# Kernel optimization log

Hardware: AMD Instinct MI355X
Metric: run time of the kernel (lower is better)

Reference implementation:

```python
import jax, jax.numpy as jnp
import numpy as np

GN_GROUPS = 32
GN_EPS = 1e-5
K = 3  # deform kernel size, padding=1, dilation=1


def conv1x1(x, w):  # x [B,C,H,W], w [O,C]
    return jnp.einsum('bchw,oc->bohw', x, w)


def conv3x3(x, w):  # w [O,I,3,3], stride 1, pad 1
    return jax.lax.conv_general_dilated(
        x, w, window_strides=(1, 1), padding=((1, 1), (1, 1)),
        dimension_numbers=('NCHW', 'OIHW', 'NCHW'))


def group_norm(x, gamma, beta):
    B, C, H, W = x.shape
    xg = x.reshape(B, GN_GROUPS, C // GN_GROUPS, H, W)
    mu = xg.mean(axis=(2, 3, 4), keepdims=True)
    var = xg.var(axis=(2, 3, 4), keepdims=True)
    xn = ((xg - mu) * jax.lax.rsqrt(var + GN_EPS)).reshape(B, C, H, W)
    return xn * gamma[None, :, None, None] + beta[None, :, None, None]


def deform_conv(x, offset, w):
    """DeformConv v1, kernel 3, pad 1, deformable_groups=1.
    x [B,C,H,W]; offset [B,18,H,W] as (dy,dx) per kernel tap; w [O,C,3,3]."""
    B, C, H, W = x.shape
    off = offset.reshape(B, K * K, 2, H, W)
    dy, dx = off[:, :, 0], off[:, :, 1]                      # [B,9,H,W]
    ky, kx = jnp.meshgrid(jnp.arange(K) - 1, jnp.arange(K) - 1, indexing='ij')
    ky = ky.reshape(1, K * K, 1, 1).astype(x.dtype)
    kx = kx.reshape(1, K * K, 1, 1).astype(x.dtype)
    gy = jnp.arange(H, dtype=x.dtype).reshape(1, 1, H, 1)
    gx = jnp.arange(W, dtype=x.dtype).reshape(1, 1, 1, W)
    py = gy + ky + dy                                        # [B,9,H,W] sample y
    px = gx + kx + dx                                        # [B,9,H,W] sample x

    y0 = jnp.floor(py); x0 = jnp.floor(px)
    wy1 = py - y0; wy0 = 1.0 - wy1
    wx1 = px - x0; wx0 = 1.0 - wx1
    xf = x.reshape(B, C, H * W)

    def corner(yc, xc, wgt):
        valid = (yc >= 0) & (yc < H) & (xc >= 0) & (xc < W)  # zero padding outside
        yi = jnp.clip(yc, 0, H - 1).astype(jnp.int32)
        xi = jnp.clip(xc, 0, W - 1).astype(jnp.int32)
        idx = (yi * W + xi).reshape(B, -1)                   # [B, 9*H*W]
        v = jax.vmap(lambda f, i: f[:, i])(xf, idx)          # [B, C, 9*H*W]
        v = v.reshape(B, C, K * K, H, W)
        return v * (wgt * valid.astype(x.dtype))[:, None]

    sampled = (corner(y0, x0, wy0 * wx0) + corner(y0, x0 + 1, wy0 * wx1)
               + corner(y0 + 1, x0, wy1 * wx0) + corner(y0 + 1, x0 + 1, wy1 * wx1))
    # contract sampled [B,C,9,H,W] with weights [O,C,9]
    return jnp.einsum('bckhw,ock->bohw', sampled, w.reshape(w.shape[0], C, K * K))


def setup_inputs() -> dict:
    key = jax.random.key(0)
    ks = jax.random.split(key, 8)
    B, Cc, H, W = 4, 256, 128, 128
    ci = Cc // 4  # 64
    x = jax.random.normal(ks[0], (B, Cc, H, W), dtype=jnp.float32)
    w1 = jax.random.normal(ks[1], (ci, Cc), dtype=jnp.float32) * 0.05
    g1 = jnp.ones((ci,), jnp.float32); b1 = jnp.zeros((ci,), jnp.float32)
    w_off = jax.random.normal(ks[2], (18, ci, 3, 3), dtype=jnp.float32) * 0.01
    w_def = jax.random.normal(ks[3], (ci, ci, 3, 3), dtype=jnp.float32) * 0.05
    w3 = jax.random.normal(ks[4], (Cc, ci), dtype=jnp.float32) * 0.05
    g3 = jnp.ones((Cc,), jnp.float32); b3 = jnp.zeros((Cc,), jnp.float32)
    return {'x': x, 'w1': w1, 'g1': g1, 'b1': b1, 'w_off': w_off,
            'w_def': w_def, 'w3': w3, 'g3': g3, 'b3': b3}


def reference(x, w1, g1, b1, w_off, w_def, w3, g3, b3):
    xd = jax.nn.relu(group_norm(conv1x1(x, w1), g1, b1))     # scale1
    offset1 = conv3x3(xd, w_off)                              # off_conva
    out1 = deform_conv(xd, offset1, w_def)                    # kernel_conva
    out = out1 + xd
    out = jax.nn.relu(group_norm(conv1x1(out, w3), g3, b3)) + x  # scale3 + residual
    return out
```

## Files before the change

### kernel.cpp

```cpp
#include <hip/hip_runtime.h>


#define HW 16384
#define WIDTH 128

typedef __attribute__((ext_vector_type(8))) short bf16x8;
typedef __attribute__((ext_vector_type(4))) float f32x4;

__device__ __forceinline__ unsigned short f2bf(float f) {
  unsigned int u = __float_as_uint(f);
  u = (u + 0x7fffu + ((u >> 16) & 1u)) >> 16;
  return (unsigned short)u;
}
__device__ __forceinline__ float bflo(unsigned int u) { return __uint_as_float(u << 16); }
__device__ __forceinline__ float bfhi(unsigned int u) { return __uint_as_float(u & 0xffff0000u); }

__global__ __launch_bounds__(256) void k_prep(const float* __restrict__ w1, const float* __restrict__ w3,
                                              const float* __restrict__ wdef, const float* __restrict__ woff,
                                              unsigned short* __restrict__ wA1f,
                                              unsigned short* __restrict__ wBf,
                                              unsigned short* __restrict__ wofBf,
                                              unsigned short* __restrict__ w3Bf) {
  int i = blockIdx.x * 256 + threadIdx.x;
  if (i < 16384) {
    int j = i & 7;
    int lane = (i >> 3) & 63;
    int m = (i >> 9) & 3;
    int kt = i >> 11;
    int o = (m << 4) + (lane & 15);
    int c = kt * 32 + ((lane >> 4) << 3) + j;
    wA1f[i] = f2bf(w1[(size_t)o * 256 + c]);
  }
  if (i < 36864) {
    int j = i & 7;
    int lane = (i >> 3) & 63;
    int n = (i >> 9) & 3;
    int kt = i >> 11;
    int kk = kt * 32 + ((lane >> 4) << 3) + j;
    int tap = kk >> 6, c = kk & 63;
    int o = (n << 4) + (lane & 15);
    wBf[i] = f2bf(wdef[(size_t)o * 576 + c * 9 + tap]);
  }
  if (i < 18432) {
    int j = i & 7;
    int lane = (i >> 3) & 63;
    int n = (i >> 9) & 1;
    int kt = i >> 10;
    int kk = kt * 32 + ((lane >> 4) << 3) + j;
    int tap = kk >> 6, c = kk & 63;
    int o = (n << 4) + (lane & 15);
    wofBf[i] = (o < 18) ? f2bf(woff[((size_t)(o * 64 + c)) * 9 + tap]) : (unsigned short)0;
  }
  if (i < 32768) {
    int j = i & 7;
    int lane = (i >> 3) & 63;
    int n = (i >> 9) & 15;
    int kt = i >> 13;
    int c = kt * 32 + ((lane >> 4) << 3) + j;
    int o = (n << 4) + (lane & 15);
    w3Bf[i] = f2bf(w3[(size_t)o * 64 + c]);
  }
}

__global__ __launch_bounds__(256) void k_conv1m(const float* __restrict__ x,
                                                const unsigned short* __restrict__ wA1f,
                                                unsigned short* __restrict__ xdT, float* __restrict__ ps) {
  __shared__ unsigned short xs[64][72];
  __shared__ float lds_s[4][32], lds_ss[4][32];
  int tid = threadIdx.x;
  int wave = tid >> 6, lane = tid & 63;
  int b = blockIdx.x >> 8;
  int chunk = blockIdx.x & 255;
  int px0 = chunk << 6;
  int pxl = lane & 15, q = lane >> 4;
  const float* xb = x + (size_t)b * 256 * HW + px0;
  const bf16x8* wAp = (const bf16x8*)wA1f;
  f32x4 acc[4];
#pragma unroll
  for (int m = 0; m < 4; m++) acc[m] = (f32x4){0.f, 0.f, 0.f, 0.f};

  for (int cb = 0; cb < 4; cb++) {
    __syncthreads();
#pragma unroll
    for (int r = 0; r < 4; r++) {
      int idx = r * 256 + tid;
      int c = idx >> 4;
      int qd = idx & 15;
      float4 v = *(const float4*)(xb + (size_t)(cb * 64 + c) * HW + qd * 4);
      xs[qd * 4 + 0][c] = f2bf(v.x);
      xs[qd * 4 + 1][c] = f2bf(v.y);
      xs[qd * 4 + 2][c] = f2bf(v.z);
      xs[qd * 4 + 3][c] = f2bf(v.w);
    }
    __syncthreads();
#pragma unroll
    for (int kt = 0; kt < 2; kt++) {
      bf16x8 bfrag = *(const bf16x8*)&xs[wave * 16 + pxl][kt * 32 + q * 8];
      int ktG = cb * 2 + kt;
#pragma unroll
      for (int m = 0; m < 4; m++) {
        bf16x8 af = wAp[(ktG * 4 + m) * 64 + lane];
        acc[m] = __builtin_amdgcn_mfma_f32_16x16x32_bf16(af, bfrag, acc[m], 0, 0, 0);
      }
    }
  }
  unsigned short* xo = xdT + ((size_t)b * HW + px0 + wave * 16 + pxl) * 64 + (q << 2);
#pragma unroll
  for (int m = 0; m < 4; m++) {
    unsigned int u0, u1;
    asm("v_cvt_pk_bf16_f32 %0, %1, %2" : "=v"(u0) : "v"(acc[m][0]), "v"(acc[m][1]));
    asm("v_cvt_pk_bf16_f32 %0, %1, %2" : "=v"(u1) : "v"(acc[m][2]), "v"(acc[m][3]));
    *(uint2*)(xo + m * 16) = make_uint2(u0, u1);
  }
  float s[8], sq[8];
#pragma unroll
  for (int m = 0; m < 4; m++)
#pragma unroll
    for (int h = 0; h < 2; h++) {
      float a = acc[m][2 * h] + acc[m][2 * h + 1];
      float qq = acc[m][2 * h] * acc[m][2 * h] + acc[m][2 * h + 1] * acc[m][2 * h + 1];
      s[m * 2 + h] = a; sq[m * 2 + h] = qq;
    }
#pragma unroll
  for (int i = 0; i < 8; i++) {
#pragma unroll
    for (int off = 8; off; off >>= 1) {
      s[i] += __shfl_down(s[i], off, 16);
      sq[i] += __shfl_down(sq[i], off, 16);
    }
  }
  if (pxl == 0) {
#pragma unroll
    for (int i = 0; i < 8; i++) {
      int m = i >> 1, h = i & 1;
      int g = m * 8 + q * 2 + h;
      lds_s[wave][g] = s[i];
      lds_ss[wave][g] = sq[i];
    }
  }
  __syncthreads();
  if (tid < 32) {
    float S = lds_s[0][tid] + lds_s[1][tid] + lds_s[2][tid] + lds_s[3][tid];
    float SS = lds_ss[0][tid] + lds_ss[1][tid] + lds_ss[2][tid] + lds_ss[3][tid];
    int bg = b * 32 + tid;
    ps[(bg * 256 + chunk) * 2] = S;
    ps[(bg * 256 + chunk) * 2 + 1] = SS;
  }
}

__global__ __launch_bounds__(256) void k_gnfin_p(const float* __restrict__ ps, float* __restrict__ mrs,
                                                 int S, float n) {
  int bg = blockIdx.x;
  float s = 0.f, ss = 0.f;
  for (int i = threadIdx.x; i < S; i += 256) { s += ps[(bg * S + i) * 2]; ss += ps[(bg * S + i) * 2 + 1]; }
#pragma unroll
  for (int off = 32; off; off >>= 1) { s += __shfl_down(s, off); ss += __shfl_down(ss, off); }
  __shared__ float ls[4], lss[4];
  int wv = threadIdx.x >> 6;
  if ((threadIdx.x & 63) == 0) { ls[wv] = s; lss[wv] = ss; }
  __syncthreads();
  if (threadIdx.x == 0) {
    float Sa = ls[0] + ls[1] + ls[2] + ls[3];
    float SSa = lss[0] + lss[1] + lss[2] + lss[3];
    float mu = Sa / n;
    float var = SSa / n - mu * mu;
    mrs[bg] = mu;
    mrs[128 + bg] = rsqrtf(var + 1e-5f);
  }
}

__global__ __launch_bounds__(256) void k_gnapply_bf(unsigned short* __restrict__ xdT,
                                                    const float* __restrict__ mrs,
                                                    const float* __restrict__ g1, const float* __restrict__ b1) {
  int i = blockIdx.x * 256 + threadIdx.x;
  int b = i >> 17;
  int ck = i & 7;
  int c0 = ck << 3;
  uint4 v = ((const uint4*)xdT)[i];
  float ga[8], be[8];
#pragma unroll
  for (int j = 0; j < 8; j += 2) {
    int g = (c0 + j) >> 1;
    float mu = mrs[b * 32 + g], rs = mrs[128 + b * 32 + g];
    ga[j] = g1[c0 + j] * rs;     be[j] = b1[c0 + j] - mu * ga[j];
    ga[j + 1] = g1[c0 + j + 1] * rs; be[j + 1] = b1[c0 + j + 1] - mu * ga[j + 1];
  }
  float r[8];
  r[0] = fmaxf(bflo(v.x) * ga[0] + be[0], 0.f);
  r[1] = fmaxf(bfhi(v.x) * ga[1] + be[1], 0.f);
  r[2] = fmaxf(bflo(v.y) * ga[2] + be[2], 0.f);
  r[3] = fmaxf(bfhi(v.y) * ga[3] + be[3], 0.f);
  r[4] = fmaxf(bflo(v.z) * ga[4] + be[4], 0.f);
  r[5] = fmaxf(bfhi(v.z) * ga[5] + be[5], 0.f);
  r[6] = fmaxf(bflo(v.w) * ga[6] + be[6], 0.f);
  r[7] = fmaxf(bfhi(v.w) * ga[7] + be[7], 0.f);
  uint4 o;
  asm("v_cvt_pk_bf16_f32 %0, %1, %2" : "=v"(o.x) : "v"(r[0]), "v"(r[1]));
  asm("v_cvt_pk_bf16_f32 %0, %1, %2" : "=v"(o.y) : "v"(r[2]), "v"(r[3]));
  asm("v_cvt_pk_bf16_f32 %0, %1, %2" : "=v"(o.z) : "v"(r[4]), "v"(r[5]));
  asm("v_cvt_pk_bf16_f32 %0, %1, %2" : "=v"(o.w) : "v"(r[6]), "v"(r[7]));
  ((uint4*)xdT)[i] = o;
}

__global__ __launch_bounds__(576, 7) void k_mega(const unsigned short* __restrict__ xdT,
                                                 const unsigned short* __restrict__ wofBf,
                                                 const unsigned short* __restrict__ wBf,
                                                 const unsigned short* __restrict__ w3Bf,
                                                 unsigned short* __restrict__ t3,
                                                 float* __restrict__ ps2) {
  __shared__ unsigned short A[36 * 65 * 8];
  __shared__ float offsL[64 * 18];
  int tid = threadIdx.x;
  int bb = blockIdx.x >> 8;
  int tileid = blockIdx.x & 255;
  int px0 = tileid << 6;
  const unsigned short* xtf = xdT + (size_t)bb * 64 * HW;
  const char* xbt = (const char*)xtf;
  int wave = tid >> 6;
  int lane = tid & 63;
  int q16 = lane >> 2;
  int ch4 = lane & 3;
  int kcbyte = (wave * 4 + ch4) * 1040;
  int kq = lane >> 4;

  f32x4 aoff = {0.f, 0.f, 0.f, 0.f};
  {
    int ky = wave / 3 - 1, kx = wave % 3 - 1;
    int n2 = wave & 1;
    int mh1 = wave >> 1;
    int r1 = mh1 * 16 + (lane & 15);
    for (int h = 0; h < 2; ++h) {
      int co = (h << 6) + (ch4 << 4);
#pragma unroll
      for (int g = 0; g < 4; ++g) {
        int src = (g << 4) + q16;
        int px = px0 + src;
        int sy = (px >> 7) + ky;
        int sx = (px & 127) + kx;
        bool valid = ((unsigned)sy < 128u) && ((unsigned)sx < 128u);
        uint4 v = make_uint4(0u, 0u, 0u, 0u);
        if (valid) v = *(const uint4*)(xbt + (((sy << 7) + sx) << 7) + co);
        *(uint4*)((char*)A + kcbyte + src * 16) = v;
      }
      __syncthreads();
      if (wave < 8) {
        const bf16x8* wp = (const bf16x8*)wofBf;
        __builtin_amdgcn_s_setprio(1);
#pragma unroll
        for (int tap = 0; tap < 9; ++tap) {
          bf16x8 bk = wp[((2 * tap + h) * 2 + n2) * 64 + lane];
          bf16x8 a0 = *(const bf16x8*)((const char*)A + ((tap * 4 + kq) * 65 + r1) * 16);
          aoff = __builtin_amdgcn_mfma_f32_16x16x32_bf16(a0, bk, aoff, 0, 0, 0);
        }
        __builtin_amdgcn_s_setprio(0);
      }
      __syncthreads();
    }
    if (wave < 8) {
      int o = n2 * 16 + (lane & 15);
      if (o < 18) {
        int prow = mh1 * 16 + ((lane >> 4) << 2);
#pragma unroll
        for (int r = 0; r < 4; r++) offsL[(prow + r) * 18 + o] = aoff[r];
      }
    }
  }
  __syncthreads();

  float w00, w01, w10, w11;
  int a00, a01, a10, a11;
  {
    int px = px0 + lane;
    int y = px >> 7, xc = px & 127;
    float dy = offsL[lane * 18 + 2 * wave];
    float dx = offsL[lane * 18 + 2 * wave + 1];
    float py = (float)(y + wave / 3 - 1) + dy;
    float pxx = (float)(xc + wave % 3 - 1) + dx;
    float y0f = floorf(py), x0f = floorf(pxx);
    float ay = py - y0f, ax = pxx - x0f;
    int y0 = (int)y0f, x0 = (int)x0f;
    int y1i = y0 + 1, x1i = x0 + 1;
    float by0 = 1.f - ay, bx0 = 1.f - ax;
    bool vy0 = (unsigned)y0 < 128u, vy1 = (unsigned)y1i < 128u;
    bool vx0 = (unsigned)x0 < 128u, vx1 = (unsigned)x1i < 128u;
    w00 = (vy0 && vx0) ? by0 * bx0 : 0.f;
    w01 = (vy0 && vx1) ? by0 * ax : 0.f;
    w10 = (vy1 && vx0) ? ay * bx0 : 0.f;
    w11 = (vy1 && vx1) ? ay * ax : 0.f;
    int iy0 = min(max(y0, 0), 127), iy1 = min(max(y1i, 0), 127);
    int ix0 = min(max(x0, 0), 127), ix1 = min(max(x1i, 0), 127);
    a00 = (iy0 * WIDTH + ix0) << 7;
    a01 = (iy0 * WIDTH + ix1) << 7;
    a10 = (iy1 * WIDTH + ix0) << 7;
    a11 = (iy1 * WIDTH + ix1) << 7;
  }

  int n1 = wave & 3;
  int mh = wave >> 2;
  f32x4 acc0 = {0.f, 0.f, 0.f, 0.f};
  f32x4 acc1 = {0.f, 0.f, 0.f, 0.f};
  for (int h = 0; h < 2; ++h) {
    int co = (h << 6) + (ch4 << 4);
#pragma unroll
    for (int g = 0; g < 4; ++g) {
      int src = (g << 4) + q16;
      float j0 = __shfl(w00, src), j1 = __shfl(w01, src);
      float j2 = __shfl(w10, src), j3 = __shfl(w11, src);
      int b0 = __shfl(a00, src), b1 = __shfl(a01, src);
      int b2 = __shfl(a10, src), b3 = __shfl(a11, src);
      uint4 v0 = *(const uint4*)(xbt + b0 + co);
      uint4 v1 = *(const uint4*)(xbt + b1 + co);
      uint4 v2 = *(const uint4*)(xbt + b2 + co);
      uint4 v3 = *(const uint4*)(xbt + b3 + co);
      float r[8];
      r[0] = j0 * bflo(v0.x) + j1 * bflo(v1.x) + j2 * bflo(v2.x) + j3 * bflo(v3.x);
      r[1] = j0 * bfhi(v0.x) + j1 * bfhi(v1.x) + j2 * bfhi(v2.x) + j3 * bfhi(v3.x);
      r[2] = j0 * bflo(v0.y) + j1 * bflo(v1.y) + j2 * bflo(v2.y) + j3 * bflo(v3.y);
      r[3] = j0 * bfhi(v0.y) + j1 * bfhi(v1.y) + j2 * bfhi(v2.y) + j3 * bfhi(v3.y);
      r[4] = j0 * bflo(v0.z) + j1 * bflo(v1.z) + j2 * bflo(v2.z) + j3 * bflo(v3.z);
      r[5] = j0 * bfhi(v0.z) + j1 * bfhi(v1.z) + j2 * bfhi(v2.z) + j3 * bfhi(v3.z);
      r[6] = j0 * bflo(v0.w) + j1 * bflo(v1.w) + j2 * bflo(v2.w) + j3 * bflo(v3.w);
      r[7] = j0 * bfhi(v0.w) + j1 * bfhi(v1.w) + j2 * bfhi(v2.w) + j3 * bfhi(v3.w);
      uint4 ov;
      asm("v_cvt_pk_bf16_f32 %0, %1, %2" : "=v"(ov.x) : "v"(r[0]), "v"(r[1]));
      asm("v_cvt_pk_bf16_f32 %0, %1, %2" : "=v"(ov.y) : "v"(r[2]), "v"(r[3]));
      asm("v_cvt_pk_bf16_f32 %0, %1, %2" : "=v"(ov.z) : "v"(r[4]), "v"(r[5]));
      asm("v_cvt_pk_bf16_f32 %0, %1, %2" : "=v"(ov.w) : "v"(r[6]), "v"(r[7]));
      *(uint4*)((char*)A + kcbyte + src * 16) = ov;
    }
    __syncthreads();
    if (wave < 8) {
      int r0r = mh * 32 + (lane & 15);
      const bf16x8* wp = (const bf16x8*)wBf;
      __builtin_amdgcn_s_setprio(1);
#pragma unroll
      for (int tap = 0; tap < 9; ++tap) {
        bf16x8 bk = wp[((2 * tap + h) * 4 + n1) * 64 + lane];
        int kc = tap * 4 + kq;
        bf16x8 a0 = *(const bf16x8*)((const char*)A + (kc * 65 + r0r) * 16);
        bf16x8 a1 = *(const bf16x8*)((const char*)A + (kc * 65 + r0r + 16) * 16);
        acc0 = __builtin_amdgcn_mfma_f32_16x16x32_bf16(a0, bk, acc0, 0, 0, 0);
        acc1 = __builtin_amdgcn_mfma_f32_16x16x32_bf16(a1, bk, acc1, 0, 0, 0);
      }
      __builtin_amdgcn_s_setprio(0);
    }
    __syncthreads();
  }
  if (wave < 8) {
    int c = n1 * 16 + (lane & 15);
    int pb = px0 + mh * 32 + ((lane >> 4) << 2);
#pragma unroll
    for (int r = 0; r < 4; r++) {
      acc0[r] += __uint_as_float((unsigned int)xtf[(size_t)(pb + r) * 64 + c] << 16);
      acc1[r] += __uint_as_float((unsigned int)xtf[(size_t)(pb + 16 + r) * 64 + c] << 16);
    }
    char* base = (char*)A + (c >> 3) * 1040 + (c & 7) * 2;
    int pxr = mh * 32 + ((lane >> 4) << 2);
#pragma unroll
    for (int r = 0; r < 4; r++) {
      *(unsigned short*)(base + (size_t)(pxr + r) * 16) = f2bf(acc0[r]);
      *(unsigned short*)(base + (size_t)(pxr + 16 + r) * 16) = f2bf(acc1[r]);
    }
  }
  __syncthreads();
  if (wave >= 8) return;

  f32x4 cA[4], cB[4];
#pragma unroll
  for (int ni = 0; ni < 4; ni++) {
    cA[ni] = (f32x4){0.f, 0.f, 0.f, 0.f};
    cB[ni] = (f32x4){0.f, 0.f, 0.f, 0.f};
  }
  {
    int mt0 = (wave >> 2) * 2;
    const bf16x8* wp2 = (const bf16x8*)w3Bf;
    __builtin_amdgcn_s_setprio(1);
#pragma unroll
    for (int kt = 0; kt < 2; kt++) {
      int kc = kt * 4 + kq;
      bf16x8 aA = *(const bf16x8*)((const char*)A + (size_t)(kc * 65 + mt0 * 16 + (lane & 15)) * 16);
      bf16x8 aB = *(const bf16x8*)((const char*)A + (size_t)(kc * 65 + (mt0 + 1) * 16 + (lane & 15)) * 16);
#pragma unroll
      for (int ni = 0; ni < 4; ni++) {
        int ng = n1 * 4 + ni;
        bf16x8 bk = wp2[(kt * 16 + ng) * 64 + lane];
        cA[ni] = __builtin_amdgcn_mfma_f32_16x16x32_bf16(aA, bk, cA[ni], 0, 0, 0);
        cB[ni] = __builtin_amdgcn_mfma_f32_16x16x32_bf16(aB, bk, cB[ni], 0, 0, 0);
      }
    }
    __builtin_amdgcn_s_setprio(0);
  }
#pragma unroll
  for (int ni = 0; ni < 4; ni++) {
    float s = 0.f, qq = 0.f;
#pragma unroll
    for (int r = 0; r < 4; r++) {
      float v0 = cA[ni][r], v1 = cB[ni][r];
      s += v0 + v1; qq += v0 * v0 + v1 * v1;
    }
    s += __shfl_down(s, 32); qq += __shfl_down(qq, 32);
    s += __shfl_down(s, 16); qq += __shfl_down(qq, 16);
    s += __shfl_down(s, 4);  qq += __shfl_down(qq, 4);
    s += __shfl_down(s, 2);  qq += __shfl_down(qq, 2);
    s += __shfl_down(s, 1);  qq += __shfl_down(qq, 1);
    if (lane == 0 || lane == 8) {
      int g = (n1 * 4 + ni) * 2 + (lane >> 3);
      int slot = ((bb * 32 + g) * 256 + tileid) * 2 + (wave >> 2);
      ps2[slot * 2] = s;
      ps2[slot * 2 + 1] = qq;
    }
  }
  unsigned short* tb = t3 + (size_t)bb * 256 * HW + px0;
  int mtq = (wave >> 2) * 32 + ((lane >> 4) << 2);
#pragma unroll
  for (int ni = 0; ni < 4; ni++) {
    int o = (n1 * 4 + ni) * 16 + (lane & 15);
    unsigned short* p0 = tb + (size_t)o * HW + mtq;
    unsigned int u0, u1, u2, u3;
    asm("v_cvt_pk_bf16_f32 %0, %1, %2" : "=v"(u0) : "v"(cA[ni][0]), "v"(cA[ni][1]));
    asm("v_cvt_pk_bf16_f32 %0, %1, %2" : "=v"(u1) : "v"(cA[ni][2]), "v"(cA[ni][3]));
    asm("v_cvt_pk_bf16_f32 %0, %1, %2" : "=v"(u2) : "v"(cB[ni][0]), "v"(cB[ni][1]));
    asm("v_cvt_pk_bf16_f32 %0, %1, %2" : "=v"(u3) : "v"(cB[ni][2]), "v"(cB[ni][3]));
    *(uint2*)p0 = make_uint2(u0, u1);
    *(uint2*)(p0 + 16) = make_uint2(u2, u3);
  }
}

__global__ __launch_bounds__(256) void k_final(const unsigned short* __restrict__ t3, const float* __restrict__ x,
                                               const float* __restrict__ mrs, const float* __restrict__ g3,
                                               const float* __restrict__ b3, float* __restrict__ out) {
  int i4 = blockIdx.x * 256 + threadIdx.x;
  int b = i4 >> 20;
  int c = (i4 >> 12) & 255;
  int g = c >> 3;
  float mu = mrs[b * 32 + g], rs = mrs[128 + b * 32 + g];
  float ga = g3[c] * rs, be = b3[c] - mu * ga;
  uint2 tv = ((const uint2*)t3)[i4];
  float t0 = bflo(tv.x);
  float t1 = bfhi(tv.x);
  float t2 = bflo(tv.y);
  float t3v = bfhi(tv.y);
  float4 xv = ((const float4*)x)[i4];
  float4 r;
  r.x = fmaxf(t0 * ga + be, 0.f) + xv.x;
  r.y = fmaxf(t1 * ga + be, 0.f) + xv.y;
  r.z = fmaxf(t2 * ga + be, 0.f) + xv.z;
  r.w = fmaxf(t3v * ga + be, 0.f) + xv.w;
  ((float4*)out)[i4] = r;
}

extern "C" void kernel_launch(void* const* d_in, const int* in_sizes, int n_in,
                              void* d_out, int out_size, void* d_ws, size_t ws_size,
                              hipStream_t stream) {
  const float* x    = (const float*)d_in[0];
  const float* w1   = (const float*)d_in[1];
  const float* g1   = (const float*)d_in[2];
  const float* b1   = (const float*)d_in[3];
  const float* woff = (const float*)d_in[4];
  const float* wdef = (const float*)d_in[5];
  const float* w3   = (const float*)d_in[6];
  const float* g3   = (const float*)d_in[7];
  const float* b3   = (const float*)d_in[8];
  float* ws = (float*)d_ws;

  unsigned short* xdT = (unsigned short*)ws;
  unsigned short* t3  = (unsigned short*)(ws + 2097152);
  float* base = ws + 2097152 + 8388608;
  float* mrs1 = base;
  float* mrs2 = mrs1 + 256;
  unsigned short* wA1f  = (unsigned short*)(mrs2 + 256);
  unsigned short* wBf   = (unsigned short*)(mrs2 + 256 + 8192);
  unsigned short* wofBf = (unsigned short*)(mrs2 + 256 + 8192 + 18432);
  unsigned short* w3Bf  = (unsigned short*)(mrs2 + 256 + 8192 + 18432 + 9216);
  float* ps   = mrs2 + 256 + 8192 + 18432 + 9216 + 16384;
  float* ps2  = ps + 65536;
  float* out  = (float*)d_out;

  hipLaunchKernelGGL(k_prep, dim3(144), dim3(256), 0, stream, w1, w3, wdef, woff, wA1f, wBf, wofBf, w3Bf);
  hipLaunchKernelGGL(k_conv1m, dim3(1024), dim3(256), 0, stream, x, wA1f, xdT, ps);
  hipLaunchKernelGGL(k_gnfin_p, dim3(128), dim3(256), 0, stream, ps, mrs1, 256, (float)(2 * HW));
  hipLaunchKernelGGL(k_gnapply_bf, dim3(2048), dim3(256), 0, stream, xdT, mrs1, g1, b1);
  hipLaunchKernelGGL(k_mega, dim3(1024), dim3(576), 0, stream, xdT, wofBf, wBf, w3Bf, t3, ps2);
  hipLaunchKernelGGL(k_gnfin_p, dim3(128), dim3(256), 0, stream, ps2, mrs2, 512, 131072.f);
  hipLaunchKernelGGL(k_final, dim3(16384), dim3(256), 0, stream, t3, x, mrs2, g3, b3, out);
}
```

Baseline: 110.9 us.

## Fuse GroupNorm1 apply into mega kernel and double-buffer conv1 input staging

Removes the separate GroupNorm-apply pass over xdT and instead applies per-channel scale, shift and ReLU on the fly wherever the mega kernel reads xdT: the 3x3 offset-conv staging, the bilinear corner samples and the residual add. This drops one full read and write of the 4x16384x64 bf16 intermediate plus a kernel launch, at the cost of extra ALU work per gathered corner. Separately, k_conv1m now double-buffers its LDS tile and prefetches the next channel block into registers while MFMAs run, which removes one barrier per iteration but raises register and LDS usage.

New measurement: 127.2 us. 1.15x slower.

```diff
diff --git a/kernel.cpp b/kernel.cpp
--- a/kernel.cpp
+++ b/kernel.cpp
@@ -65,7 +65,7 @@
 __global__ __launch_bounds__(256) void k_conv1m(const float* __restrict__ x,
                                                 const unsigned short* __restrict__ wA1f,
                                                 unsigned short* __restrict__ xdT, float* __restrict__ ps) {
-  __shared__ unsigned short xs[64][72];
+  __shared__ unsigned short xs[2][64][72];
   __shared__ float lds_s[4][32], lds_ss[4][32];
   int tid = threadIdx.x;
   int wave = tid >> 6, lane = tid & 63;
@@ -75,27 +75,36 @@
   int pxl = lane & 15, q = lane >> 4;
   const float* xb = x + (size_t)b * 256 * HW + px0;
   const bf16x8* wAp = (const bf16x8*)wA1f;
+  int sc = tid >> 4;
+  int sq = tid & 15;
   f32x4 acc[4];
 #pragma unroll
   for (int m = 0; m < 4; m++) acc[m] = (f32x4){0.f, 0.f, 0.f, 0.f};
 
+  float4 vr[4];
+#pragma unroll
+  for (int r = 0; r < 4; r++)
+    vr[r] = *(const float4*)(xb + (size_t)(r * 16 + sc) * HW + sq * 4);
+#pragma unroll
+  for (int r = 0; r < 4; r++) {
+    int c = r * 16 + sc;
+    xs[0][sq * 4 + 0][c] = f2bf(vr[r].x);
+    xs[0][sq * 4 + 1][c] = f2bf(vr[r].y);
+    xs[0][sq * 4 + 2][c] = f2bf(vr[r].z);
+    xs[0][sq * 4 + 3][c] = f2bf(vr[r].w);
+  }
+  __syncthreads();
+
   for (int cb = 0; cb < 4; cb++) {
-    __syncthreads();
-#pragma unroll
-    for (int r = 0; r < 4; r++) {
-      int idx = r * 256 + tid;
-      int c = idx >> 4;
-      int qd = idx & 15;
-      float4 v = *(const float4*)(xb + (size_t)(cb * 64 + c) * HW + qd * 4);
-      xs[qd * 4 + 0][c] = f2bf(v.x);
-      xs[qd * 4 + 1][c] = f2bf(v.y);
-      xs[qd * 4 + 2][c] = f2bf(v.z);
-      xs[qd * 4 + 3][c] = f2bf(v.w);
-    }
-    __syncthreads();
+    int cur = cb & 1;
+    if (cb < 3) {
+#pragma unroll
+      for (int r = 0; r < 4; r++)
+        vr[r] = *(const float4*)(xb + (size_t)((cb + 1) * 64 + r * 16 + sc) * HW + sq * 4);
+    }
 #pragma unroll
     for (int kt = 0; kt < 2; kt++) {
-      bf16x8 bfrag = *(const bf16x8*)&xs[wave * 16 + pxl][kt * 32 + q * 8];
+      bf16x8 bfrag = *(const bf16x8*)&xs[cur][wave * 16 + pxl][kt * 32 + q * 8];
       int ktG = cb * 2 + kt;
 #pragma unroll
       for (int m = 0; m < 4; m++) {
@@ -103,6 +112,17 @@
         acc[m] = __builtin_amdgcn_mfma_f32_16x16x32_bf16(af, bfrag, acc[m], 0, 0, 0);
       }
     }
+    if (cb < 3) {
+#pragma unroll
+      for (int r = 0; r < 4; r++) {
+        int c = r * 16 + sc;
+        xs[cur ^ 1][sq * 4 + 0][c] = f2bf(vr[r].x);
+        xs[cur ^ 1][sq * 4 + 1][c] = f2bf(vr[r].y);
+        xs[cur ^ 1][sq * 4 + 2][c] = f2bf(vr[r].z);
+        xs[cur ^ 1][sq * 4 + 3][c] = f2bf(vr[r].w);
+      }
+    }
+    __syncthreads();
   }
   unsigned short* xo = xdT + ((size_t)b * HW + px0 + wave * 16 + pxl) * 64 + (q << 2);
 #pragma unroll
@@ -112,21 +132,21 @@
     asm("v_cvt_pk_bf16_f32 %0, %1, %2" : "=v"(u1) : "v"(acc[m][2]), "v"(acc[m][3]));
     *(uint2*)(xo + m * 16) = make_uint2(u0, u1);
   }
-  float s[8], sq[8];
+  float s[8], sq2[8];
 #pragma unroll
   for (int m = 0; m < 4; m++)
 #pragma unroll
     for (int h = 0; h < 2; h++) {
       float a = acc[m][2 * h] + acc[m][2 * h + 1];
       float qq = acc[m][2 * h] * acc[m][2 * h] + acc[m][2 * h + 1] * acc[m][2 * h + 1];
-      s[m * 2 + h] = a; sq[m * 2 + h] = qq;
+      s[m * 2 + h] = a; sq2[m * 2 + h] = qq;
     }
 #pragma unroll
   for (int i = 0; i < 8; i++) {
 #pragma unroll
     for (int off = 8; off; off >>= 1) {
       s[i] += __shfl_down(s[i], off, 16);
-      sq[i] += __shfl_down(sq[i], off, 16);
+      sq2[i] += __shfl_down(sq2[i], off, 16);
     }
   }
   if (pxl == 0) {
@@ -135,7 +155,7 @@
       int m = i >> 1, h = i & 1;
       int g = m * 8 + q * 2 + h;
       lds_s[wave][g] = s[i];
-      lds_ss[wave][g] = sq[i];
+      lds_ss[wave][g] = sq2[i];
     }
   }
   __syncthreads();
@@ -169,47 +189,18 @@
   }
 }
 
-__global__ __launch_bounds__(256) void k_gnapply_bf(unsigned short* __restrict__ xdT,
-                                                    const float* __restrict__ mrs,
-                                                    const float* __restrict__ g1, const float* __restrict__ b1) {
-  int i = blockIdx.x * 256 + threadIdx.x;
-  int b = i >> 17;
-  int ck = i & 7;
-  int c0 = ck << 3;
-  uint4 v = ((const uint4*)xdT)[i];
-  float ga[8], be[8];
-#pragma unroll
-  for (int j = 0; j < 8; j += 2) {
-    int g = (c0 + j) >> 1;
-    float mu = mrs[b * 32 + g], rs = mrs[128 + b * 32 + g];
-    ga[j] = g1[c0 + j] * rs;     be[j] = b1[c0 + j] - mu * ga[j];
-    ga[j + 1] = g1[c0 + j + 1] * rs; be[j + 1] = b1[c0 + j + 1] - mu * ga[j + 1];
-  }
-  float r[8];
-  r[0] = fmaxf(bflo(v.x) * ga[0] + be[0], 0.f);
-  r[1] = fmaxf(bfhi(v.x) * ga[1] + be[1], 0.f);
-  r[2] = fmaxf(bflo(v.y) * ga[2] + be[2], 0.f);
-  r[3] = fmaxf(bfhi(v.y) * ga[3] + be[3], 0.f);
-  r[4] = fmaxf(bflo(v.z) * ga[4] + be[4], 0.f);
-  r[5] = fmaxf(bfhi(v.z) * ga[5] + be[5], 0.f);
-  r[6] = fmaxf(bflo(v.w) * ga[6] + be[6], 0.f);
-  r[7] = fmaxf(bfhi(v.w) * ga[7] + be[7], 0.f);
-  uint4 o;
-  asm("v_cvt_pk_bf16_f32 %0, %1, %2" : "=v"(o.x) : "v"(r[0]), "v"(r[1]));
-  asm("v_cvt_pk_bf16_f32 %0, %1, %2" : "=v"(o.y) : "v"(r[2]), "v"(r[3]));
-  asm("v_cvt_pk_bf16_f32 %0, %1, %2" : "=v"(o.z) : "v"(r[4]), "v"(r[5]));
-  asm("v_cvt_pk_bf16_f32 %0, %1, %2" : "=v"(o.w) : "v"(r[6]), "v"(r[7]));
-  ((uint4*)xdT)[i] = o;
-}
-
 __global__ __launch_bounds__(576, 7) void k_mega(const unsigned short* __restrict__ xdT,
                                                  const unsigned short* __restrict__ wofBf,
                                                  const unsigned short* __restrict__ wBf,
                                                  const unsigned short* __restrict__ w3Bf,
+                                                 const float* __restrict__ mrs,
+                                                 const float* __restrict__ g1,
+                                                 const float* __restrict__ b1,
                                                  unsigned short* __restrict__ t3,
                                                  float* __restrict__ ps2) {
   __shared__ unsigned short A[36 * 65 * 8];
   __shared__ float offsL[64 * 18];
+  __shared__ float gnc[128];
   int tid = threadIdx.x;
   int bb = blockIdx.x >> 8;
   int tileid = blockIdx.x & 255;
@@ -223,6 +214,15 @@
   int kcbyte = (wave * 4 + ch4) * 1040;
   int kq = lane >> 4;
 
+  if (tid < 64) {
+    int c = tid, g = c >> 1;
+    float mu = mrs[bb * 32 + g], rs = mrs[128 + bb * 32 + g];
+    float ga = g1[c] * rs;
+    gnc[c] = ga;
+    gnc[64 + c] = b1[c] - mu * ga;
+  }
+  __syncthreads();
+
   f32x4 aoff = {0.f, 0.f, 0.f, 0.f};
   {
     int ky = wave / 3 - 1, kx = wave % 3 - 1;
@@ -230,6 +230,11 @@
     int mh1 = wave >> 1;
     int r1 = mh1 * 16 + (lane & 15);
     for (int h = 0; h < 2; ++h) {
+      int c0 = (h << 5) + (ch4 << 3);
+      float4 gA = *(const float4*)&gnc[c0];
+      float4 gB = *(const float4*)&gnc[c0 + 4];
+      float4 bA = *(const float4*)&gnc[64 + c0];
+      float4 bB = *(const float4*)&gnc[64 + c0 + 4];
       int co = (h << 6) + (ch4 << 4);
 #pragma unroll
       for (int g = 0; g < 4; ++g) {
@@ -240,7 +245,21 @@
         bool valid = ((unsigned)sy < 128u) && ((unsigned)sx < 128u);
         uint4 v = make_uint4(0u, 0u, 0u, 0u);
         if (valid) v = *(const uint4*)(xbt + (((sy << 7) + sx) << 7) + co);
-        *(uint4*)((char*)A + kcbyte + src * 16) = v;
+        float r[8];
+        r[0] = valid ? fmaxf(bflo(v.x) * gA.x + bA.x, 0.f) : 0.f;
+        r[1] = valid ? fmaxf(bfhi(v.x) * gA.y + bA.y, 0.f) : 0.f;
+        r[2] = valid ? fmaxf(bflo(v.y) * gA.z + bA.z, 0.f) : 0.f;
+        r[3] = valid ? fmaxf(bfhi(v.y) * gA.w + bA.w, 0.f) : 0.f;
+        r[4] = valid ? fmaxf(bflo(v.z) * gB.x + bB.x, 0.f) : 0.f;
+        r[5] = valid ? fmaxf(bfhi(v.z) * gB.y + bB.y, 0.f) : 0.f;
+        r[6] = valid ? fmaxf(bflo(v.w) * gB.z + bB.z, 0.f) : 0.f;
+        r[7] = valid ? fmaxf(bfhi(v.w) * gB.w + bB.w, 0.f) : 0.f;
+        uint4 ov;
+        asm("v_cvt_pk_bf16_f32 %0, %1, %2" : "=v"(ov.x) : "v"(r[0]), "v"(r[1]));
+        asm("v_cvt_pk_bf16_f32 %0, %1, %2" : "=v"(ov.y) : "v"(r[2]), "v"(r[3]));
+        asm("v_cvt_pk_bf16_f32 %0, %1, %2" : "=v"(ov.z) : "v"(r[4]), "v"(r[5]));
+        asm("v_cvt_pk_bf16_f32 %0, %1, %2" : "=v"(ov.w) : "v"(r[6]), "v"(r[7]));
+        *(uint4*)((char*)A + kcbyte + src * 16) = ov;
       }
       __syncthreads();
       if (wave < 8) {
@@ -300,27 +319,42 @@
   f32x4 acc0 = {0.f, 0.f, 0.f, 0.f};
   f32x4 acc1 = {0.f, 0.f, 0.f, 0.f};
   for (int h = 0; h < 2; ++h) {
+    int c0 = (h << 5) + (ch4 << 3);
+    float4 gA = *(const float4*)&gnc[c0];
+    float4 gB = *(const float4*)&gnc[c0 + 4];
+    float4 bA = *(const float4*)&gnc[64 + c0];
+    float4 bB = *(const float4*)&gnc[64 + c0 + 4];
     int co = (h << 6) + (ch4 << 4);
 #pragma unroll
     for (int g = 0; g < 4; ++g) {
       int src = (g << 4) + q16;
       float j0 = __shfl(w00, src), j1 = __shfl(w01, src);
       float j2 = __shfl(w10, src), j3 = __shfl(w11, src);
-      int b0 = __shfl(a00, src), b1 = __shfl(a01, src);
-      int b2 = __shfl(a10, src), b3 = __shfl(a11, src);
+      int b0 = __shfl(a00, src), b1v = __shfl(a01, src);
+      int b2 = __shfl(a10, src), b3v = __shfl(a11, src);
       uint4 v0 = *(const uint4*)(xbt + b0 + co);
-      uint4 v1 = *(const uint4*)(xbt + b1 + co);
+      uint4 v1 = *(const uint4*)(xbt + b1v + co);
       uint4 v2 = *(const uint4*)(xbt + b2 + co);
-      uint4 v3 = *(const uint4*)(xbt + b3 + co);
+      uint4 v3 = *(const uint4*)(xbt + b3v + co);
       float r[8];
-      r[0] = j0 * bflo(v0.x) + j1 * bflo(v1.x) + j2 * bflo(v2.x) + j3 * bflo(v3.x);
-      r[1] = j0 * bfhi(v0.x) + j1 * bfhi(v1.x) + j2 * bfhi(v2.x) + j3 * bfhi(v3.x);
-      r[2] = j0 * bflo(v0.y) + j1 * bflo(v1.y) + j2 * bflo(v2.y) + j3 * bflo(v3.y);
-      r[3] = j0 * bfhi(v0.y) + j1 * bfhi(v1.y) + j2 * bfhi(v2.y) + j3 * bfhi(v3.y);
-      r[4] = j0 * bflo(v0.z) + j1 * bflo(v1.z) + j2 * bflo(v2.z) + j3 * bflo(v3.z);
-      r[5] = j0 * bfhi(v0.z) + j1 * bfhi(v1.z) + j2 * bfhi(v2.z) + j3 * bfhi(v3.z);
-      r[6] = j0 * bflo(v0.w) + j1 * bflo(v1.w) + j2 * bflo(v2.w) + j3 * bflo(v3.w);
-      r[7] = j0 * bfhi(v0.w) + j1 * bfhi(v1.w) + j2 * bfhi(v2.w) + j3 * bfhi(v3.w);
+#define CORNER(UV, GAc, BEc) fmaxf((UV) * (GAc) + (BEc), 0.f)
+      r[0] = j0 * CORNER(bflo(v0.x), gA.x, bA.x) + j1 * CORNER(bflo(v1.x), gA.x, bA.x)
+           + j2 * CORNER(bflo(v2.x), gA.x, bA.x) + j3 * CORNER(bflo(v3.x), gA.x, bA.x);
+      r[1] = j0 * CORNER(bfhi(v0.x), gA.y, bA.y) + j1 * CORNER(bfhi(v1.x), gA.y, bA.y)
+           + j2 * CORNER(bfhi(v2.x), gA.y, bA.y) + j3 * CORNER(bfhi(v3.x), gA.y, bA.y);
+      r[2] = j0 * CORNER(bflo(v0.y), gA.z, bA.z) + j1 * CORNER(bflo(v1.y), gA.z, bA.z)
+           + j2 * CORNER(bflo(v2.y), gA.z, bA.z) + j3 * CORNER(bflo(v3.y), gA.z, bA.z);
+      r[3] = j0 * CORNER(bfhi(v0.y), gA.w, bA.w) + j1 * CORNER(bfhi(v1.y), gA.w, bA.w)
+           + j2 * CORNER(bfhi(v2.y), gA.w, bA.w) + j3 * CORNER(bfhi(v3.y), gA.w, bA.w);
+      r[4] = j0 * CORNER(bflo(v0.z), gB.x, bB.x) + j1 * CORNER(bflo(v1.z), gB.x, bB.x)
+           + j2 * CORNER(bflo(v2.z), gB.x, bB.x) + j3 * CORNER(bflo(v3.z), gB.x, bB.x);
+      r[5] = j0 * CORNER(bfhi(v0.z), gB.y, bB.y) + j1 * CORNER(bfhi(v1.z), gB.y, bB.y)
+           + j2 * CORNER(bfhi(v2.z), gB.y, bB.y) + j3 * CORNER(bfhi(v3.z), gB.y, bB.y);
+      r[6] = j0 * CORNER(bflo(v0.w), gB.z, bB.z) + j1 * CORNER(bflo(v1.w), gB.z, bB.z)
+           + j2 * CORNER(bflo(v2.w), gB.z, bB.z) + j3 * CORNER(bflo(v3.w), gB.z, bB.z);
+      r[7] = j0 * CORNER(bfhi(v0.w), gB.w, bB.w) + j1 * CORNER(bfhi(v1.w), gB.w, bB.w)
+           + j2 * CORNER(bfhi(v2.w), gB.w, bB.w) + j3 * CORNER(bfhi(v3.w), gB.w, bB.w);
+#undef CORNER
       uint4 ov;
       asm("v_cvt_pk_bf16_f32 %0, %1, %2" : "=v"(ov.x) : "v"(r[0]), "v"(r[1]));
       asm("v_cvt_pk_bf16_f32 %0, %1, %2" : "=v"(ov.y) : "v"(r[2]), "v"(r[3]));
@@ -348,11 +382,14 @@
   }
   if (wave < 8) {
     int c = n1 * 16 + (lane & 15);
+    float ga_r = gnc[c], be_r = gnc[64 + c];
     int pb = px0 + mh * 32 + ((lane >> 4) << 2);
 #pragma unroll
     for (int r = 0; r < 4; r++) {
-      acc0[r] += __uint_as_float((unsigned int)xtf[(size_t)(pb + r) * 64 + c] << 16);
-      acc1[r] += __uint_as_float((unsigned int)xtf[(size_t)(pb + 16 + r) * 64 + c] << 16);
+      float v0 = __uint_as_float((unsigned int)xtf[(size_t)(pb + r) * 64 + c] << 16);
+      float v1 = __uint_as_float((unsigned int)xtf[(size_t)(pb + 16 + r) * 64 + c] << 16);
+      acc0[r] += fmaxf(v0 * ga_r + be_r, 0.f);
+      acc1[r] += fmaxf(v1 * ga_r + be_r, 0.f);
     }
     char* base = (char*)A + (c >> 3) * 1040 + (c & 7) * 2;
     int pxr = mh * 32 + ((lane >> 4) << 2);
@@ -479,8 +516,7 @@
   hipLaunchKernelGGL(k_prep, dim3(144), dim3(256), 0, stream, w1, w3, wdef, woff, wA1f, wBf, wofBf, w3Bf);
   hipLaunchKernelGGL(k_conv1m, dim3(1024), dim3(256), 0, stream, x, wA1f, xdT, ps);
   hipLaunchKernelGGL(k_gnfin_p, dim3(128), dim3(256), 0, stream, ps, mrs1, 256, (float)(2 * HW));
-  hipLaunchKernelGGL(k_gnapply_bf, dim3(2048), dim3(256), 0, stream, xdT, mrs1, g1, b1);
-  hipLaunchKernelGGL(k_mega, dim3(1024), dim3(576), 0, stream, xdT, wofBf, wBf, w3Bf, t3, ps2);
+  hipLaunchKernelGGL(k_mega, dim3(1024), dim3(576), 0, stream, xdT, wofBf, wBf, w3Bf, mrs1, g1, b1, t3, ps2);
   hipLaunchKernelGGL(k_gnfin_p, dim3(128), dim3(256), 0, stream, ps2, mrs2, 512, 131072.f);
   hipLaunchKernelGGL(k_final, dim3(16384), dim3(256), 0, stream, t3, x, mrs2, g3, b3, out);
 }
```
